# Performance work log

Measured on AMD Instinct MI355X. Metric: run time of the kernel, lower is better.

## Reference

```python
import jax, jax.numpy as jnp
import numpy as np

NH = 32
LN_EPS = 1e-5

def _mlp2(x, w1, b1, w2, b2):
    # Linear -> ReLU -> Linear (torch convention: y = x @ W^T + b)
    return jnp.maximum(x @ w1.T + b1, 0.0) @ w2.T + b2

def _layernorm(x, g, b):
    m = x.mean(-1, keepdims=True)
    v = jnp.mean((x - m) ** 2, axis=-1, keepdims=True)
    return (x - m) / jnp.sqrt(v + LN_EPS) * g + b

def _pos_enc(pos):
    # P[..., 2i] = sin(pos/(i+1)*pi), P[..., 2i+1] = cos(pos/(i+1)*pi)
    i = jnp.arange(NH // 2, dtype=pos.dtype)
    ang = pos[..., None] * (jnp.pi / (i + 1.0))  # [B, L, NH/2]
    return jnp.stack([jnp.sin(ang), jnp.cos(ang)], axis=-1).reshape(pos.shape[0], pos.shape[1], NH)

def _forward(x0, x1, pos0, pos1, xcT,
             e0w1, e0b1, e0w2, e0b2,
             e1w1, e1b1, e1w2, e1b2,
             ecw1, ecb1, ecw2, ecb2,
             wq, wk, wv, wo,
             ln1g, ln1b, ln2g, ln2b,
             f1w1, f1b1, f1w2, f1b2,
             f2w1, f2b1, f2w2, f2b2,
             l0, l1):
    # InputFeature
    e0 = _mlp2(x0, e0w1, e0b1, e0w2, e0b2) + _pos_enc(pos0)      # [B, l0, 32]
    e1 = _mlp2(x1, e1w1, e1b1, e1w2, e1b2) + _pos_enc(pos1)      # [B, l1, 32]
    ec = _mlp2(xcT, ecw1, ecb1, ecw2, ecb2)                      # [B, 32]
    xIn = jnp.concatenate([e0, e1, ec[:, None, :]], axis=1)      # [B, L, 32], L = l0+l1+1
    # AttentionLayer: attention over the feature axis (faithful to bmm(q^T, k))
    q = xIn @ wq.T; k = xIn @ wk.T; v = xIn @ wv.T               # [B, L, 32]
    L = xIn.shape[1]
    score = jnp.einsum('blh,blg->bhg', q, k) / jnp.sqrt(jnp.asarray(L, xIn.dtype))  # [B, 32, 32]
    att = jax.nn.softmax(score, axis=-1)
    a = jnp.einsum('bhg,blg->blh', att, v) @ wo.T                # [B, L, 32]
    # addnorm1 (dropout in eval = identity) + ffn1 + addnorm2 + ffn2
    h1 = _layernorm(a + xIn, ln1g, ln1b)
    h2 = _mlp2(h1, f1w1, f1b1, f1w2, f1b2)
    h3 = _layernorm(h2 + xIn, ln2g, ln2b)
    y = _mlp2(h3, f2w1, f2b1, f2w2, f2b2)[..., 0]                # [B, L]
    # segment-mean pooling: sum of per-segment means (last segment = xc token)
    return y[:, :l0].mean(-1) + y[:, l0:l0 + l1].mean(-1) + y[:, l0 + l1:].mean(-1)

def setup_inputs() -> dict:
    key = jax.random.key(0)
    ks = iter(jax.random.split(key, 48))
    B, L0, L1, N0, N1, NXC = 2048, 365, 366, 8, 16, 32
    lin = lambda o, i: jax.random.normal(next(ks), (o, i), jnp.float32) * np.float32(1.0 / np.sqrt(i))
    d = {}
    d['x0'] = jax.random.normal(next(ks), (B, L0, N0), jnp.float32)
    d['x1'] = jax.random.normal(next(ks), (B, L1, N1), jnp.float32)
    d['pos0'] = jax.random.uniform(next(ks), (B, L0), jnp.float32) * 365.0
    d['pos1'] = jax.random.uniform(next(ks), (B, L1), jnp.float32) * 365.0
    d['xcT'] = jax.random.normal(next(ks), (B, NXC), jnp.float32)
    d['e0w1'] = lin(NH, N0); d['e0b1'] = jnp.zeros((NH,), jnp.float32)
    d['e0w2'] = lin(NH, NH); d['e0b2'] = jnp.zeros((NH,), jnp.float32)
    d['e1w1'] = lin(NH, N1); d['e1b1'] = jnp.zeros((NH,), jnp.float32)
    d['e1w2'] = lin(NH, NH); d['e1b2'] = jnp.zeros((NH,), jnp.float32)
    d['ecw1'] = lin(NH, NXC); d['ecb1'] = jnp.zeros((NH,), jnp.float32)
    d['ecw2'] = lin(NH, NH); d['ecb2'] = jnp.zeros((NH,), jnp.float32)
    d['wq'] = lin(NH, NH); d['wk'] = lin(NH, NH); d['wv'] = lin(NH, NH); d['wo'] = lin(NH, NH)
    d['ln1g'] = jnp.ones((NH,), jnp.float32); d['ln1b'] = jnp.zeros((NH,), jnp.float32)
    d['ln2g'] = jnp.ones((NH,), jnp.float32); d['ln2b'] = jnp.zeros((NH,), jnp.float32)
    d['f1w1'] = lin(NH, NH); d['f1b1'] = jnp.zeros((NH,), jnp.float32)
    d['f1w2'] = lin(NH, NH); d['f1b2'] = jnp.zeros((NH,), jnp.float32)
    d['f2w1'] = lin(NH, NH); d['f2b1'] = jnp.zeros((NH,), jnp.float32)
    d['f2w2'] = lin(1, NH); d['f2b2'] = jnp.zeros((1,), jnp.float32)
    d['l0'] = L0; d['l1'] = L1
    return d

def reference(x0, x1, pos0, pos1, xcT,
              e0w1, e0b1, e0w2, e0b2, e1w1, e1b1, e1w2, e1b2,
              ecw1, ecb1, ecw2, ecb2, wq, wk, wv, wo,
              ln1g, ln1b, ln2g, ln2b,
              f1w1, f1b1, f1w2, f1b2, f2w1, f2b1, f2w2, f2b2,
              l0, l1):
    return _forward(x0, x1, pos0, pos1, xcT,
                    e0w1, e0b1, e0w2, e0b2, e1w1, e1b1, e1w2, e1b2,
                    ecw1, ecb1, ecw2, ecb2, wq, wk, wv, wo,
                    ln1g, ln1b, ln2g, ln2b,
                    f1w1, f1b1, f1w2, f1b2, f2w1, f2b1, f2w2, f2b2,
                    l0, l1)
```

## Files before the change

kernel.cpp:

```cpp
#include <hip/hip_runtime.h>
#include <math.h>

#define L0T 365
#define L1T 366
#define LT  732
#define NTILE 46
#define NW   4
#define NTHR 256
#define PI_F 3.14159265358979323846f

typedef short svec8 __attribute__((ext_vector_type(8)));
typedef float fvec4 __attribute__((ext_vector_type(4)));
typedef float fvec16 __attribute__((ext_vector_type(16)));
typedef unsigned uvec4 __attribute__((ext_vector_type(4)));

__device__ __forceinline__ unsigned short f2bf(float f) {
    unsigned u = __float_as_uint(f);
    u = (u + 0x7fffu + ((u >> 16) & 1u)) >> 16;
    return (unsigned short)u;
}
__device__ __forceinline__ float bf2f(unsigned short s) {
    return __uint_as_float(((unsigned)s) << 16);
}
__device__ __forceinline__ unsigned pk2(float a, float b) {
    return (unsigned)f2bf(a) | ((unsigned)f2bf(b) << 16);
}
__device__ __forceinline__ unsigned cvtpk(float a, float b) {
    unsigned r;
    asm("v_cvt_pk_bf16_f32 %0, %1, %2" : "=v"(r) : "v"(a), "v"(b));
    return r;
}
__device__ __forceinline__ float pgetv(uvec4 p, int j) {
    unsigned u = p[j >> 1];
    return bf2f((unsigned short)((j & 1) ? (u >> 16) : (u & 0xffffu)));
}
__device__ __forceinline__ svec8 pack8(float4 a, float4 c) {
    uvec4 u;
    u[0] = cvtpk(a.x, a.y); u[1] = cvtpk(a.z, a.w);
    u[2] = cvtpk(c.x, c.y); u[3] = cvtpk(c.z, c.w);
    return __builtin_bit_cast(svec8, u);
}

__device__ __forceinline__ void embed_pass(
    const unsigned short* __restrict__ T1,
    const unsigned short* __restrict__ T2,
    const float* __restrict__ Bh, const float* __restrict__ Bx,
    svec8 bx, int ln, int Q, float* __restrict__ out)
{
    svec8 w1f0 = *(const svec8*)&T1[ln * 8];
    svec8 w1f1 = *(const svec8*)&T1[512 + ln * 8];
    const fvec4* bh = (const fvec4*)&Bh[Q * 8];
    fvec4 d0 = __builtin_amdgcn_mfma_f32_16x16x32_bf16(w1f0, bx, bh[0], 0, 0, 0);
    fvec4 d1 = __builtin_amdgcn_mfma_f32_16x16x32_bf16(w1f1, bx, bh[1], 0, 0, 0);
    uvec4 hu;
    hu[0] = cvtpk(fmaxf(d0[0], 0.f), fmaxf(d0[1], 0.f));
    hu[1] = cvtpk(fmaxf(d0[2], 0.f), fmaxf(d0[3], 0.f));
    hu[2] = cvtpk(fmaxf(d1[0], 0.f), fmaxf(d1[1], 0.f));
    hu[3] = cvtpk(fmaxf(d1[2], 0.f), fmaxf(d1[3], 0.f));
    svec8 hf = __builtin_bit_cast(svec8, hu);
    svec8 w2f0 = *(const svec8*)&T2[ln * 8];
    svec8 w2f1 = *(const svec8*)&T2[512 + ln * 8];
    const fvec4* bb = (const fvec4*)&Bx[Q * 8];
    fvec4 g0 = __builtin_amdgcn_mfma_f32_16x16x32_bf16(w2f0, hf, bb[0], 0, 0, 0);
    fvec4 g1 = __builtin_amdgcn_mfma_f32_16x16x32_bf16(w2f1, hf, bb[1], 0, 0, 0);
    out[0] = g0[0]; out[1] = g0[1]; out[2] = g0[2]; out[3] = g0[3];
    out[4] = g1[0]; out[5] = g1[1]; out[6] = g1[2]; out[7] = g1[3];
}

__device__ __forceinline__ void embed_tile(
    int t, int b, int tk, int Q, int ln,
    const float* __restrict__ x0, const float* __restrict__ x1,
    const float* __restrict__ pos0, const float* __restrict__ pos1,
    const unsigned short* __restrict__ TBL,
    const float* __restrict__ BIA,
    float4 pwr,
    const float* __restrict__ ECV,
    float* __restrict__ xv)
{
    const float pwa[4] = {pwr.x, pwr.y, pwr.z, pwr.w};
    const int tok = t * 16 + tk;
    if (t < 22) {
        svec8 bx;
        #pragma unroll
        for (int j = 0; j < 8; j++) bx[j] = 0;
        if (Q == 0) {
            const float4* px = (const float4*)(x0 + ((size_t)b * L0T + tok) * 8);
            bx = pack8(px[0], px[1]);
        }
        embed_pass(TBL, TBL + 1024, BIA, BIA + 32, bx, ln, Q, xv);
        float pv = pos0[(size_t)b * L0T + tok];
        #pragma unroll
        for (int j = 0; j < 8; j += 2) {
            float s, c; __sincosf(pv * pwa[j >> 1], &s, &c);
            xv[j] += s; xv[j + 1] += c;
        }
    } else if (t == 22) {
        float ea[8], eb[8];
        svec8 bx0, bx1;
        #pragma unroll
        for (int j = 0; j < 8; j++) { bx0[j] = 0; bx1[j] = 0; }
        if (Q == 0 && tok < L0T) {
            const float4* px = (const float4*)(x0 + ((size_t)b * L0T + tok) * 8);
            bx0 = pack8(px[0], px[1]);
        }
        if (Q < 2 && tok >= L0T) {
            const float4* px = (const float4*)(x1 + ((size_t)b * L1T + (tok - L0T)) * 16 + Q * 8);
            bx1 = pack8(px[0], px[1]);
        }
        embed_pass(TBL,        TBL + 1024, BIA,      BIA + 32, bx0, ln, Q, ea);
        embed_pass(TBL + 2048, TBL + 3072, BIA + 64, BIA + 96, bx1, ln, Q, eb);
        float pv = (tok < L0T) ? pos0[(size_t)b * L0T + tok]
                               : pos1[(size_t)b * L1T + (tok - L0T)];
        #pragma unroll
        for (int j = 0; j < 8; j += 2) {
            float s, c; __sincosf(pv * pwa[j >> 1], &s, &c);
            xv[j]     = ((tok < L0T) ? ea[j]     : eb[j])     + s;
            xv[j + 1] = ((tok < L0T) ? ea[j + 1] : eb[j + 1]) + c;
        }
    } else if (t < 45) {
        svec8 bx;
        #pragma unroll
        for (int j = 0; j < 8; j++) bx[j] = 0;
        if (Q < 2) {
            const float4* px = (const float4*)(x1 + ((size_t)b * L1T + (tok - L0T)) * 16 + Q * 8);
            bx = pack8(px[0], px[1]);
        }
        embed_pass(TBL + 2048, TBL + 3072, BIA + 64, BIA + 96, bx, ln, Q, xv);
        float pv = pos1[(size_t)b * L1T + (tok - L0T)];
        #pragma unroll
        for (int j = 0; j < 8; j += 2) {
            float s, c; __sincosf(pv * pwa[j >> 1], &s, &c);
            xv[j] += s; xv[j + 1] += c;
        }
    } else {
        float ea[8];
        svec8 bx1;
        #pragma unroll
        for (int j = 0; j < 8; j++) bx1[j] = 0;
        if (Q < 2 && tok <= LT - 2) {
            const float4* px = (const float4*)(x1 + ((size_t)b * L1T + (tok - L0T)) * 16 + Q * 8);
            bx1 = pack8(px[0], px[1]);
        }
        embed_pass(TBL + 2048, TBL + 3072, BIA + 64, BIA + 96, bx1, ln, Q, ea);
        float pv = (tok <= LT - 2) ? pos1[(size_t)b * L1T + (tok - L0T)] : 0.f;
        #pragma unroll
        for (int j = 0; j < 8; j += 2) {
            float s, c; __sincosf(pv * pwa[j >> 1], &s, &c);
            xv[j]     = (tok <= LT - 2) ? ea[j] + s
                        : ((tok == LT - 1) ? ECV[Q * 8 + j] : 0.f);
            xv[j + 1] = (tok <= LT - 2) ? ea[j + 1] + c
                        : ((tok == LT - 1) ? ECV[Q * 8 + j + 1] : 0.f);
        }
    }
}

__global__ __launch_bounds__(NTHR, 6) void fused_kernel(
    const float* __restrict__ x0,  const float* __restrict__ x1,
    const float* __restrict__ pos0,const float* __restrict__ pos1,
    const float* __restrict__ xcT,
    const float* __restrict__ e0w1,const float* __restrict__ e0b1,
    const float* __restrict__ e0w2,const float* __restrict__ e0b2,
    const float* __restrict__ e1w1,const float* __restrict__ e1b1,
    const float* __restrict__ e1w2,const float* __restrict__ e1b2,
    const float* __restrict__ ecw1,const float* __restrict__ ecb1,
    const float* __restrict__ ecw2,const float* __restrict__ ecb2,
    const float* __restrict__ wq,  const float* __restrict__ wk,
    const float* __restrict__ wv,  const float* __restrict__ wo,
    const float* __restrict__ ln1g,const float* __restrict__ ln1b,
    const float* __restrict__ ln2g,const float* __restrict__ ln2b,
    const float* __restrict__ f1w1,const float* __restrict__ f1b1,
    const float* __restrict__ f1w2,const float* __restrict__ f1b2,
    const float* __restrict__ f2w1,const float* __restrict__ f2b1,
    const float* __restrict__ f2w2,const float* __restrict__ f2b2,
    float* __restrict__ out)
{
    const int b   = blockIdx.x;
    const int tid = threadIdx.x;
    const int w   = tid >> 6;
    const int ln  = tid & 63;
    const int tk  = ln & 15;
    const int Q   = ln >> 4;
    const int Lr0 = ((tk >> 2) * 8) + (tk & 3);
    const int Lr1 = Lr0 + 4;

    __shared__ unsigned short TBL[4 * 1024] __attribute__((aligned(16)));
    __shared__ float BIA[128] __attribute__((aligned(16)));
    __shared__ unsigned PCK[128] __attribute__((aligned(16)));
    __shared__ float T1f[1024] __attribute__((aligned(16)));
    __shared__ float CmT2[1024] __attribute__((aligned(16)));
    __shared__ unsigned short Wbb[1024] __attribute__((aligned(16)));
    __shared__ float ECV[32] __attribute__((aligned(16)));
    __shared__ float red[NW * 3];

    float4 pwr;
    pwr.x = PI_F / (float)(Q * 4 + 1);
    pwr.y = PI_F / (float)(Q * 4 + 2);
    pwr.z = PI_F / (float)(Q * 4 + 3);
    pwr.w = PI_F / (float)(Q * 4 + 4);

    for (int idx = tid; idx < 1024; idx += NTHR) {
        int f = idx >> 9, lane = (idx >> 3) & 63, j = idx & 7;
        int tkk = lane & 15, QQ = lane >> 4;
        int Lr = ((tkk >> 2) * 8) + (tkk & 3) + f * 4;
        int col = QQ * 8 + j;
        TBL[idx]        = (col < 8)  ? f2bf(e0w1[Lr * 8  + col]) : (unsigned short)0;
        TBL[1024 + idx] = f2bf(e0w2[Lr * 32 + col]);
        TBL[2048 + idx] = (col < 16) ? f2bf(e1w1[Lr * 16 + col]) : (unsigned short)0;
        TBL[3072 + idx] = f2bf(e1w2[Lr * 32 + col]);
        CmT2[idx] = 0.f;
    }
    if (tid < 128) {
        int s = tid >> 5, i = tid & 31;
        float bv;
        if      (s == 0) bv = e0b1[i];
        else if (s == 1) bv = e0b2[i];
        else if (s == 2) bv = e1b1[i];
        else             bv = e1b2[i];
        BIA[tid] = bv;
    }
    if (tid < 128) {
        int t8 = tid >> 4, q = (tid >> 2) & 3, i = tid & 3, f = q * 8 + 2 * i;
        const float* sp;
        if      (t8 == 0) sp = ln1g;
        else if (t8 == 1) sp = ln1b;
        else if (t8 == 2) sp = ln2g;
        else if (t8 == 3) sp = ln2b;
        else if (t8 == 4) sp = f1b1;
        else if (t8 == 5) sp = f1b2;
        else if (t8 == 6) sp = f2b1;
        else              sp = f2w2;
        PCK[tid] = pk2(sp[f], sp[f + 1]);
    }
    float* ECH = T1f;
    if (tid >= 224) {
        int i = tid - 224;
        const float4* xr = (const float4*)(xcT + (size_t)b * 32);
        const float4* wr = (const float4*)&ecw1[i * 32];
        float a = ecb1[i];
        #pragma unroll
        for (int j4 = 0; j4 < 8; j4++) {
            float4 ww = wr[j4], xx = xr[j4];
            a = fmaf(ww.x, xx.x, a); a = fmaf(ww.y, xx.y, a);
            a = fmaf(ww.z, xx.z, a); a = fmaf(ww.w, xx.w, a);
        }
        ECH[i] = fmaxf(a, 0.f);
    }
    __syncthreads();
    if (tid >= 224) {
        int i = tid - 224;
        const float4* wr = (const float4*)&ecw2[i * 32];
        float a = ecb2[i];
        #pragma unroll
        for (int j4 = 0; j4 < 8; j4++) {
            float4 ww = wr[j4];
            a = fmaf(ww.x, ECH[j4 * 4 + 0], a); a = fmaf(ww.y, ECH[j4 * 4 + 1], a);
            a = fmaf(ww.z, ECH[j4 * 4 + 2], a); a = fmaf(ww.w, ECH[j4 * 4 + 3], a);
        }
        ECV[i] = a;
    }
    __syncthreads();

    {
        unsigned short* ST = (unsigned short*)T1f;
        const int feat = ln & 31, half = ln >> 5;
        fvec16 dG;
        #pragma unroll
        for (int i = 0; i < 16; i++) dG[i] = 0.f;
        for (int t = w; t < NTILE; t += NW) {
            float xv[8];
            embed_tile(t, b, tk, Q, ln, x0, x1, pos0, pos1, TBL, BIA, pwr, ECV, xv);
            uvec4 pk;
            pk[0] = cvtpk(xv[0], xv[1]); pk[1] = cvtpk(xv[2], xv[3]);
            pk[2] = cvtpk(xv[4], xv[5]); pk[3] = cvtpk(xv[6], xv[7]);
            *(uvec4*)&ST[(w * 16 + tk) * 32 + Q * 8] = pk;
            svec8 af;
            #pragma unroll
            for (int j = 0; j < 8; j++)
                af[j] = (short)ST[w * 512 + (half * 8 + j) * 32 + feat];
            dG = __builtin_amdgcn_mfma_f32_32x32x16_bf16(af, af, dG, 0, 0, 0);
        }
        #pragma unroll
        for (int rg = 0; rg < 16; rg++) {
            int row = (rg & 3) + 8 * (rg >> 2) + 4 * half;
            atomicAdd(&CmT2[row * 32 + feat], dG[rg]);
        }
    }
    __syncthreads();

    for (int idx = tid; idx < 1024; idx += NTHR) {
        int i = idx >> 5, g = idx & 31;
        const float4* cr = (const float4*)&CmT2[i * 32];
        const float4* wr = (const float4*)&wk[g * 32];
        float a = 0.f;
        #pragma unroll
        for (int j4 = 0; j4 < 8; j4++) {
            float4 cc = cr[j4], ww = wr[j4];
            a = fmaf(cc.x, ww.x, a); a = fmaf(cc.y, ww.y, a);
            a = fmaf(cc.z, ww.z, a); a = fmaf(cc.w, ww.w, a);
        }
        T1f[idx] = a;
    }
    __syncthreads();
    const float rsL = rsqrtf((float)LT);
    for (int idx = tid; idx < 1024; idx += NTHR) {
        int h = idx >> 5, g = idx & 31;
        const float4* qr = (const float4*)&wq[h * 32];
        float a = 0.f;
        #pragma unroll
        for (int i4 = 0; i4 < 8; i4++) {
            float4 qq = qr[i4];
            a = fmaf(qq.x, T1f[(i4 * 4 + 0) * 32 + g], a);
            a = fmaf(qq.y, T1f[(i4 * 4 + 1) * 32 + g], a);
            a = fmaf(qq.z, T1f[(i4 * 4 + 2) * 32 + g], a);
            a = fmaf(qq.w, T1f[(i4 * 4 + 3) * 32 + g], a);
        }
        CmT2[idx] = a * rsL;
    }
    __syncthreads();
    {
        int r = tid >> 3, c0 = (tid & 7) * 4;
        float4 vv = *(const float4*)&CmT2[r * 32 + c0];
        float m = fmaxf(fmaxf(vv.x, vv.y), fmaxf(vv.z, vv.w));
        m = fmaxf(m, __shfl_xor(m, 1));
        m = fmaxf(m, __shfl_xor(m, 2));
        m = fmaxf(m, __shfl_xor(m, 4));
        float ex = __expf(vv.x - m), ey = __expf(vv.y - m);
        float ez = __expf(vv.z - m), ew = __expf(vv.w - m);
        float s = ex + ey + ez + ew;
        s += __shfl_xor(s, 1); s += __shfl_xor(s, 2); s += __shfl_xor(s, 4);
        float inv = 1.f / s;
        float4 o; o.x = ex * inv; o.y = ey * inv; o.z = ez * inv; o.w = ew * inv;
        *(float4*)&CmT2[r * 32 + c0] = o;
    }
    __syncthreads();
    for (int idx = tid; idx < 1024; idx += NTHR) {
        int h = idx >> 5, j = idx & 31;
        const float4* pr = (const float4*)&CmT2[h * 32];
        float a = 0.f;
        #pragma unroll
        for (int g4 = 0; g4 < 8; g4++) {
            float4 pp = pr[g4];
            a = fmaf(pp.x, wv[(g4 * 4 + 0) * 32 + j], a);
            a = fmaf(pp.y, wv[(g4 * 4 + 1) * 32 + j], a);
            a = fmaf(pp.z, wv[(g4 * 4 + 2) * 32 + j], a);
            a = fmaf(pp.w, wv[(g4 * 4 + 3) * 32 + j], a);
        }
        T1f[idx] = a;
    }
    __syncthreads();
    for (int idx = tid; idx < 1024; idx += NTHR) {
        int o = idx >> 5, j = idx & 31;
        const float4* orow = (const float4*)&wo[o * 32];
        float a = 0.f;
        #pragma unroll
        for (int h4 = 0; h4 < 8; h4++) {
            float4 oo = orow[h4];
            a = fmaf(oo.x, T1f[(h4 * 4 + 0) * 32 + j], a);
            a = fmaf(oo.y, T1f[(h4 * 4 + 1) * 32 + j], a);
            a = fmaf(oo.z, T1f[(h4 * 4 + 2) * 32 + j], a);
            a = fmaf(oo.w, T1f[(h4 * 4 + 3) * 32 + j], a);
        }
        Wbb[idx] = f2bf(a + (o == j ? 1.f : 0.f));
    }
    __syncthreads();

    svec8 wbf0 = *(const svec8*)&Wbb[Lr0 * 32 + Q * 8];
    svec8 wbf1 = *(const svec8*)&Wbb[Lr1 * 32 + Q * 8];
    svec8 a1f0, a1f1, a2f0, a2f1, a3f0, a3f1;
    #pragma unroll
    for (int j = 0; j < 8; j++) {
        a1f0[j] = (short)f2bf(f1w1[Lr0 * 32 + Q * 8 + j]);
        a1f1[j] = (short)f2bf(f1w1[Lr1 * 32 + Q * 8 + j]);
        a2f0[j] = (short)f2bf(f1w2[Lr0 * 32 + Q * 8 + j]);
        a2f1[j] = (short)f2bf(f1w2[Lr1 * 32 + Q * 8 + j]);
        a3f0[j] = (short)f2bf(f2w1[Lr0 * 32 + Q * 8 + j]);
        a3f1[j] = (short)f2bf(f2w1[Lr1 * 32 + Q * 8 + j]);
    }
    const float ybias = f2b2[0];
    const fvec4 zc = {0.f, 0.f, 0.f, 0.f};

    float s0 = 0.f, s1 = 0.f, s2 = 0.f;
    for (int t = w; t < NTILE; t += NW) {
        float xv[8];
        embed_tile(t, b, tk, Q, ln, x0, x1, pos0, pos1, TBL, BIA, pwr, ECV, xv);
        uvec4 pkx;
        pkx[0] = cvtpk(xv[0], xv[1]); pkx[1] = cvtpk(xv[2], xv[3]);
        pkx[2] = cvtpk(xv[4], xv[5]); pkx[3] = cvtpk(xv[6], xv[7]);
        svec8 bx = __builtin_bit_cast(svec8, pkx);

        const uvec4* P4 = (const uvec4*)PCK;
        uvec4 pg1 = P4[Q],      pb1 = P4[4 + Q];
        uvec4 pg2 = P4[8 + Q],  pb2 = P4[12 + Q];
        uvec4 pc1 = P4[16 + Q], pc2 = P4[20 + Q];
        uvec4 pc3 = P4[24 + Q], pw2 = P4[28 + Q];

        fvec4 d0 = __builtin_amdgcn_mfma_f32_16x16x32_bf16(wbf0, bx, zc, 0, 0, 0);
        fvec4 d1 = __builtin_amdgcn_mfma_f32_16x16x32_bf16(wbf1, bx, zc, 0, 0, 0);
        float v[8];
        #pragma unroll
        for (int j = 0; j < 4; j++) { v[j] = d0[j]; v[4 + j] = d1[j]; }
        float S = 0.f, Sq = 0.f;
        #pragma unroll
        for (int j = 0; j < 8; j++) { S += v[j]; Sq = fmaf(v[j], v[j], Sq); }
        S  += __shfl_xor(S, 16);  Sq += __shfl_xor(Sq, 16);
        S  += __shfl_xor(S, 32);  Sq += __shfl_xor(Sq, 32);
        float mean = S * (1.f / 32.f);
        float var = fmaxf(Sq * (1.f / 32.f) - mean * mean, 0.f);
        float rs = rsqrtf(var + 1e-5f);
        float n[8];
        #pragma unroll
        for (int j = 0; j < 8; j++)
            n[j] = (v[j] - mean) * rs * pgetv(pg1, j) + pgetv(pb1, j);
        uvec4 tu;
        tu[0] = cvtpk(n[0], n[1]); tu[1] = cvtpk(n[2], n[3]);
        tu[2] = cvtpk(n[4], n[5]); tu[3] = cvtpk(n[6], n[7]);
        svec8 tf = __builtin_bit_cast(svec8, tu);
        fvec4 u0 = __builtin_amdgcn_mfma_f32_16x16x32_bf16(a1f0, tf, zc, 0, 0, 0);
        fvec4 u1 = __builtin_amdgcn_mfma_f32_16x16x32_bf16(a1f1, tf, zc, 0, 0, 0);
        uvec4 uu;
        uu[0] = cvtpk(fmaxf(u0[0] + pgetv(pc1, 0), 0.f), fmaxf(u0[1] + pgetv(pc1, 1), 0.f));
        uu[1] = cvtpk(fmaxf(u0[2] + pgetv(pc1, 2), 0.f), fmaxf(u0[3] + pgetv(pc1, 3), 0.f));
        uu[2] = cvtpk(fmaxf(u1[0] + pgetv(pc1, 4), 0.f), fmaxf(u1[1] + pgetv(pc1, 5), 0.f));
        uu[3] = cvtpk(fmaxf(u1[2] + pgetv(pc1, 6), 0.f), fmaxf(u1[3] + pgetv(pc1, 7), 0.f));
        svec8 uf = __builtin_bit_cast(svec8, uu);
        fvec4 g0 = __builtin_amdgcn_mfma_f32_16x16x32_bf16(a2f0, uf, zc, 0, 0, 0);
        fvec4 g1 = __builtin_amdgcn_mfma_f32_16x16x32_bf16(a2f1, uf, zc, 0, 0, 0);
        #pragma unroll
        for (int j = 0; j < 8; j++)
            v[j] = (j < 4 ? g0[j] : g1[j - 4]) + pgetv(pc2, j) + xv[j];
        float S2 = 0.f, Sq2 = 0.f;
        #pragma unroll
        for (int j = 0; j < 8; j++) { S2 += v[j]; Sq2 = fmaf(v[j], v[j], Sq2); }
        S2  += __shfl_xor(S2, 16);  Sq2 += __shfl_xor(Sq2, 16);
        S2  += __shfl_xor(S2, 32);  Sq2 += __shfl_xor(Sq2, 32);
        float mean2 = S2 * (1.f / 32.f);
        float var2 = fmaxf(Sq2 * (1.f / 32.f) - mean2 * mean2, 0.f);
        float rs2 = rsqrtf(var2 + 1e-5f);
        float n2[8];
        #pragma unroll
        for (int j = 0; j < 8; j++)
            n2[j] = (v[j] - mean2) * rs2 * pgetv(pg2, j) + pgetv(pb2, j);
        uvec4 t2u;
        t2u[0] = cvtpk(n2[0], n2[1]); t2u[1] = cvtpk(n2[2], n2[3]);
        t2u[2] = cvtpk(n2[4], n2[5]); t2u[3] = cvtpk(n2[6], n2[7]);
        svec8 t2 = __builtin_bit_cast(svec8, t2u);
        fvec4 q0 = __builtin_amdgcn_mfma_f32_16x16x32_bf16(a3f0, t2, zc, 0, 0, 0);
        fvec4 q1 = __builtin_amdgcn_mfma_f32_16x16x32_bf16(a3f1, t2, zc, 0, 0, 0);
        float yp = 0.f;
        #pragma unroll
        for (int j = 0; j < 8; j++) {
            float e = (j < 4 ? q0[j] : q1[j - 4]) + pgetv(pc3, j);
            yp = fmaf(pgetv(pw2, j), fmaxf(e, 0.f), yp);
        }
        yp += __shfl_xor(yp, 16); yp += __shfl_xor(yp, 32);
        if (Q == 0) {
            int tok = t * 16 + tk;
            float yv = yp + ybias;
            if (tok < L0T)            s0 += yv;
            else if (tok < LT - 1)    s1 += yv;
            else if (tok == LT - 1)   s2 += yv;
        }
    }

    s0 += __shfl_xor(s0, 1); s0 += __shfl_xor(s0, 2);
    s0 += __shfl_xor(s0, 4); s0 += __shfl_xor(s0, 8);
    s1 += __shfl_xor(s1, 1); s1 += __shfl_xor(s1, 2);
    s1 += __shfl_xor(s1, 4); s1 += __shfl_xor(s1, 8);
    s2 += __shfl_xor(s2, 1); s2 += __shfl_xor(s2, 2);
    s2 += __shfl_xor(s2, 4); s2 += __shfl_xor(s2, 8);
    if (ln == 0) { red[w * 3] = s0; red[w * 3 + 1] = s1; red[w * 3 + 2] = s2; }
    __syncthreads();
    if (tid == 0) {
        float a0 = 0.f, a1 = 0.f, a2 = 0.f;
        #pragma unroll
        for (int k = 0; k < NW; k++) {
            a0 += red[k * 3]; a1 += red[k * 3 + 1]; a2 += red[k * 3 + 2];
        }
        out[b] = a0 / (float)L0T + a1 / (float)L1T + a2;
    }
}

extern "C" void kernel_launch(void* const* d_in, const int* in_sizes, int n_in,
                              void* d_out, int out_size, void* d_ws, size_t ws_size,
                              hipStream_t stream)
{
    const float* x0   = (const float*)d_in[0];
    const float* x1   = (const float*)d_in[1];
    const float* pos0 = (const float*)d_in[2];
    const float* pos1 = (const float*)d_in[3];
    const float* xcT  = (const float*)d_in[4];
    const float* e0w1 = (const float*)d_in[5];
    const float* e0b1 = (const float*)d_in[6];
    const float* e0w2 = (const float*)d_in[7];
    const float* e0b2 = (const float*)d_in[8];
    const float* e1w1 = (const float*)d_in[9];
    const float* e1b1 = (const float*)d_in[10];
    const float* e1w2 = (const float*)d_in[11];
    const float* e1b2 = (const float*)d_in[12];
    const float* ecw1 = (const float*)d_in[13];
    const float* ecb1 = (const float*)d_in[14];
    const float* ecw2 = (const float*)d_in[15];
    const float* ecb2 = (const float*)d_in[16];
    const float* wq   = (const float*)d_in[17];
    const float* wk   = (const float*)d_in[18];
    const float* wv   = (const float*)d_in[19];
    const float* wo   = (const float*)d_in[20];
    const float* ln1g = (const float*)d_in[21];
    const float* ln1b = (const float*)d_in[22];
    const float* ln2g = (const float*)d_in[23];
    const float* ln2b = (const float*)d_in[24];
    const float* f1w1 = (const float*)d_in[25];
    const float* f1b1 = (const float*)d_in[26];
    const float* f1w2 = (const float*)d_in[27];
    const float* f1b2 = (const float*)d_in[28];
    const float* f2w1 = (const float*)d_in[29];
    const float* f2b1 = (const float*)d_in[30];
    const float* f2w2 = (const float*)d_in[31];
    const float* f2b2 = (const float*)d_in[32];
    float* out = (float*)d_out;

    const int B = in_sizes[0] / (L0T * 8);

    hipLaunchKernelGGL(fused_kernel, dim3(B), dim3(NTHR), 0, stream,
                       x0, x1, pos0, pos1, xcT,
                       e0w1, e0b1, e0w2, e0b2, e1w1, e1b1, e1w2, e1b2,
                       ecw1, ecb1, ecw2, ecb2, wq, wk, wv, wo,
                       ln1g, ln1b, ln2g, ln2b,
                       f1w1, f1b1, f1w2, f1b2, f2w1, f2b1, f2w2, f2b2,
                       out);
}
```

Baseline: 325.2 us.

## Split token tiles per segment and process two tiles per iteration for ILP

Re-tiles the token axis so each 16-token tile belongs to one segment (x0 or x1, with the xc token placed at the end of segment 1). This removes the mixed boundary tile that ran both embedding MLPs. Both the Gram pass and the main per-token pipeline now handle two tiles per loop iteration, issuing loads and MFMA chains side by side so their latencies can overlap; the Gram pass uses two accumulators. Occupancy in launch bounds drops from 6 to 4 to make room for the extra registers, which may reduce latency hiding across waves.

```diff
diff --git a/kernel.cpp b/kernel.cpp
--- a/kernel.cpp
+++ b/kernel.cpp
@@ -5,6 +5,7 @@
 #define L1T 366
 #define LT  732
 #define NTILE 46
+#define NSEG 23
 #define NW   4
 #define NTHR 256
 #define PI_F 3.14159265358979323846f
@@ -67,94 +68,47 @@
     out[4] = g1[0]; out[5] = g1[1]; out[6] = g1[2]; out[7] = g1[3];
 }
 
-__device__ __forceinline__ void embed_tile(
-    int t, int b, int tk, int Q, int ln,
+__device__ __forceinline__ void load_tile(
+    int t, int b, int tk, int Q,
     const float* __restrict__ x0, const float* __restrict__ x1,
     const float* __restrict__ pos0, const float* __restrict__ pos1,
-    const unsigned short* __restrict__ TBL,
-    const float* __restrict__ BIA,
-    float4 pwr,
-    const float* __restrict__ ECV,
-    float* __restrict__ xv)
+    svec8& bx, float& pv, int& seg, int& tl)
 {
+    seg = (t >= NSEG) ? 1 : 0;
+    tl  = (seg ? (t - NSEG) : t) * 16 + tk;
+    const int lim = seg ? L1T : L0T;
+    const bool tvalid = tl < lim;
+    #pragma unroll
+    for (int j = 0; j < 8; j++) bx[j] = 0;
+    const bool ld = tvalid && (seg ? (Q < 2) : (Q == 0));
+    if (ld) {
+        const float4* px = seg
+            ? (const float4*)(x1 + ((size_t)b * L1T + tl) * 16 + Q * 8)
+            : (const float4*)(x0 + ((size_t)b * L0T + tl) * 8);
+        bx = pack8(px[0], px[1]);
+    }
+    pv = 0.f;
+    if (tvalid) pv = seg ? pos1[(size_t)b * L1T + tl] : pos0[(size_t)b * L0T + tl];
+}
+
+__device__ __forceinline__ void finish_xv(
+    int seg, int tl, int Q, const float* __restrict__ e, float pv, float4 pwr,
+    const float* __restrict__ ECV, float* __restrict__ xv)
+{
+    const int lim = seg ? L1T : L0T;
+    const bool tvalid = tl < lim;
+    const bool isxc = seg && (tl == L1T);
     const float pwa[4] = {pwr.x, pwr.y, pwr.z, pwr.w};
-    const int tok = t * 16 + tk;
-    if (t < 22) {
-        svec8 bx;
-        #pragma unroll
-        for (int j = 0; j < 8; j++) bx[j] = 0;
-        if (Q == 0) {
-            const float4* px = (const float4*)(x0 + ((size_t)b * L0T + tok) * 8);
-            bx = pack8(px[0], px[1]);
-        }
-        embed_pass(TBL, TBL + 1024, BIA, BIA + 32, bx, ln, Q, xv);
-        float pv = pos0[(size_t)b * L0T + tok];
-        #pragma unroll
-        for (int j = 0; j < 8; j += 2) {
-            float s, c; __sincosf(pv * pwa[j >> 1], &s, &c);
-            xv[j] += s; xv[j + 1] += c;
-        }
-    } else if (t == 22) {
-        float ea[8], eb[8];
-        svec8 bx0, bx1;
-        #pragma unroll
-        for (int j = 0; j < 8; j++) { bx0[j] = 0; bx1[j] = 0; }
-        if (Q == 0 && tok < L0T) {
-            const float4* px = (const float4*)(x0 + ((size_t)b * L0T + tok) * 8);
-            bx0 = pack8(px[0], px[1]);
-        }
-        if (Q < 2 && tok >= L0T) {
-            const float4* px = (const float4*)(x1 + ((size_t)b * L1T + (tok - L0T)) * 16 + Q * 8);
-            bx1 = pack8(px[0], px[1]);
-        }
-        embed_pass(TBL,        TBL + 1024, BIA,      BIA + 32, bx0, ln, Q, ea);
-        embed_pass(TBL + 2048, TBL + 3072, BIA + 64, BIA + 96, bx1, ln, Q, eb);
-        float pv = (tok < L0T) ? pos0[(size_t)b * L0T + tok]
-                               : pos1[(size_t)b * L1T + (tok - L0T)];
-        #pragma unroll
-        for (int j = 0; j < 8; j += 2) {
-            float s, c; __sincosf(pv * pwa[j >> 1], &s, &c);
-            xv[j]     = ((tok < L0T) ? ea[j]     : eb[j])     + s;
-            xv[j + 1] = ((tok < L0T) ? ea[j + 1] : eb[j + 1]) + c;
-        }
-    } else if (t < 45) {
-        svec8 bx;
-        #pragma unroll
-        for (int j = 0; j < 8; j++) bx[j] = 0;
-        if (Q < 2) {
-            const float4* px = (const float4*)(x1 + ((size_t)b * L1T + (tok - L0T)) * 16 + Q * 8);
-            bx = pack8(px[0], px[1]);
-        }
-        embed_pass(TBL + 2048, TBL + 3072, BIA + 64, BIA + 96, bx, ln, Q, xv);
-        float pv = pos1[(size_t)b * L1T + (tok - L0T)];
-        #pragma unroll
-        for (int j = 0; j < 8; j += 2) {
-            float s, c; __sincosf(pv * pwa[j >> 1], &s, &c);
-            xv[j] += s; xv[j + 1] += c;
-        }
-    } else {
-        float ea[8];
-        svec8 bx1;
-        #pragma unroll
-        for (int j = 0; j < 8; j++) bx1[j] = 0;
-        if (Q < 2 && tok <= LT - 2) {
-            const float4* px = (const float4*)(x1 + ((size_t)b * L1T + (tok - L0T)) * 16 + Q * 8);
-            bx1 = pack8(px[0], px[1]);
-        }
-        embed_pass(TBL + 2048, TBL + 3072, BIA + 64, BIA + 96, bx1, ln, Q, ea);
-        float pv = (tok <= LT - 2) ? pos1[(size_t)b * L1T + (tok - L0T)] : 0.f;
-        #pragma unroll
-        for (int j = 0; j < 8; j += 2) {
-            float s, c; __sincosf(pv * pwa[j >> 1], &s, &c);
-            xv[j]     = (tok <= LT - 2) ? ea[j] + s
-                        : ((tok == LT - 1) ? ECV[Q * 8 + j] : 0.f);
-            xv[j + 1] = (tok <= LT - 2) ? ea[j + 1] + c
-                        : ((tok == LT - 1) ? ECV[Q * 8 + j + 1] : 0.f);
-        }
-    }
-}
-
-__global__ __launch_bounds__(NTHR, 6) void fused_kernel(
+    #pragma unroll
+    for (int j = 0; j < 8; j += 2) {
+        float s, c; __sincosf(pv * pwa[j >> 1], &s, &c);
+        float a0 = e[j] + s, a1 = e[j + 1] + c;
+        xv[j]     = tvalid ? a0 : (isxc ? ECV[Q * 8 + j]     : 0.f);
+        xv[j + 1] = tvalid ? a1 : (isxc ? ECV[Q * 8 + j + 1] : 0.f);
+    }
+}
+
+__global__ __launch_bounds__(NTHR, 4) void fused_kernel(
     const float* __restrict__ x0,  const float* __restrict__ x1,
     const float* __restrict__ pos0,const float* __restrict__ pos1,
     const float* __restrict__ xcT,
@@ -186,11 +140,13 @@
     __shared__ unsigned short TBL[4 * 1024] __attribute__((aligned(16)));
     __shared__ float BIA[128] __attribute__((aligned(16)));
     __shared__ unsigned PCK[128] __attribute__((aligned(16)));
-    __shared__ float T1f[1024] __attribute__((aligned(16)));
-    __shared__ float CmT2[1024] __attribute__((aligned(16)));
+    __shared__ float SCR[2048] __attribute__((aligned(16)));
     __shared__ unsigned short Wbb[1024] __attribute__((aligned(16)));
     __shared__ float ECV[32] __attribute__((aligned(16)));
     __shared__ float red[NW * 3];
+
+    float* T1f  = SCR;
+    float* CmT2 = SCR + 1024;
 
     float4 pwr;
     pwr.x = PI_F / (float)(Q * 4 + 1);
@@ -260,15 +216,21 @@
     }
     __syncthreads();
 
+    const int cnt = (NTILE - 1 - w) / NW + 1;
+
     {
         unsigned short* ST = (unsigned short*)T1f;
         const int feat = ln & 31, half = ln >> 5;
-        fvec16 dG;
-        #pragma unroll
-        for (int i = 0; i < 16; i++) dG[i] = 0.f;
-        for (int t = w; t < NTILE; t += NW) {
-            float xv[8];
-            embed_tile(t, b, tk, Q, ln, x0, x1, pos0, pos1, TBL, BIA, pwr, ECV, xv);
+        fvec16 dGA, dGB;
+        #pragma unroll
+        for (int i = 0; i < 16; i++) { dGA[i] = 0.f; dGB[i] = 0.f; }
+
+        auto embed_core = [&](int seg, svec8 bx, float* e) {
+            const unsigned short* T = TBL + seg * 2048;
+            const float* Bb = BIA + seg * 64;
+            embed_pass(T, T + 1024, Bb, Bb + 32, bx, ln, Q, e);
+        };
+        auto gram_step = [&](const float* xv, fvec16& dG) {
             uvec4 pk;
             pk[0] = cvtpk(xv[0], xv[1]); pk[1] = cvtpk(xv[2], xv[3]);
             pk[2] = cvtpk(xv[4], xv[5]); pk[3] = cvtpk(xv[6], xv[7]);
@@ -278,11 +240,36 @@
             for (int j = 0; j < 8; j++)
                 af[j] = (short)ST[w * 512 + (half * 8 + j) * 32 + feat];
             dG = __builtin_amdgcn_mfma_f32_32x32x16_bf16(af, af, dG, 0, 0, 0);
-        }
+        };
+        auto g_one = [&](int t) {
+            svec8 bx; float pv; int seg, tl;
+            load_tile(t, b, tk, Q, x0, x1, pos0, pos1, bx, pv, seg, tl);
+            float e[8]; embed_core(seg, bx, e);
+            float xv[8]; finish_xv(seg, tl, Q, e, pv, pwr, ECV, xv);
+            gram_step(xv, dGA);
+        };
+        auto g_pair = [&](int tA, int tB) {
+            svec8 bxA, bxB; float pvA, pvB; int segA, tlA, segB, tlB;
+            load_tile(tA, b, tk, Q, x0, x1, pos0, pos1, bxA, pvA, segA, tlA);
+            load_tile(tB, b, tk, Q, x0, x1, pos0, pos1, bxB, pvB, segB, tlB);
+            float eA[8], eB[8];
+            embed_core(segA, bxA, eA);
+            embed_core(segB, bxB, eB);
+            float xvA[8], xvB[8];
+            finish_xv(segA, tlA, Q, eA, pvA, pwr, ECV, xvA);
+            finish_xv(segB, tlB, Q, eB, pvB, pwr, ECV, xvB);
+            gram_step(xvA, dGA);
+            gram_step(xvB, dGB);
+        };
+
+        int ts = w;
+        if (cnt & 1) { g_one(ts); ts += NW; }
+        for (int t = ts; t < NTILE; t += 2 * NW) g_pair(t, t + NW);
+
         #pragma unroll
         for (int rg = 0; rg < 16; rg++) {
             int row = (rg & 3) + 8 * (rg >> 2) + 4 * half;
-            atomicAdd(&CmT2[row * 32 + feat], dG[rg]);
+            atomicAdd(&CmT2[row * 32 + feat], dGA[rg] + dGB[rg]);
         }
     }
     __syncthreads();
@@ -378,88 +365,122 @@
     }
     const float ybias = f2b2[0];
     const fvec4 zc = {0.f, 0.f, 0.f, 0.f};
+    const uvec4* P4 = (const uvec4*)PCK;
 
     float s0 = 0.f, s1 = 0.f, s2 = 0.f;
-    for (int t = w; t < NTILE; t += NW) {
-        float xv[8];
-        embed_tile(t, b, tk, Q, ln, x0, x1, pos0, pos1, TBL, BIA, pwr, ECV, xv);
-        uvec4 pkx;
-        pkx[0] = cvtpk(xv[0], xv[1]); pkx[1] = cvtpk(xv[2], xv[3]);
-        pkx[2] = cvtpk(xv[4], xv[5]); pkx[3] = cvtpk(xv[6], xv[7]);
-        svec8 bx = __builtin_bit_cast(svec8, pkx);
-
-        const uvec4* P4 = (const uvec4*)PCK;
-        uvec4 pg1 = P4[Q],      pb1 = P4[4 + Q];
-        uvec4 pg2 = P4[8 + Q],  pb2 = P4[12 + Q];
-        uvec4 pc1 = P4[16 + Q], pc2 = P4[20 + Q];
-        uvec4 pc3 = P4[24 + Q], pw2 = P4[28 + Q];
-
-        fvec4 d0 = __builtin_amdgcn_mfma_f32_16x16x32_bf16(wbf0, bx, zc, 0, 0, 0);
-        fvec4 d1 = __builtin_amdgcn_mfma_f32_16x16x32_bf16(wbf1, bx, zc, 0, 0, 0);
-        float v[8];
-        #pragma unroll
-        for (int j = 0; j < 4; j++) { v[j] = d0[j]; v[4 + j] = d1[j]; }
-        float S = 0.f, Sq = 0.f;
-        #pragma unroll
-        for (int j = 0; j < 8; j++) { S += v[j]; Sq = fmaf(v[j], v[j], Sq); }
-        S  += __shfl_xor(S, 16);  Sq += __shfl_xor(Sq, 16);
-        S  += __shfl_xor(S, 32);  Sq += __shfl_xor(Sq, 32);
-        float mean = S * (1.f / 32.f);
-        float var = fmaxf(Sq * (1.f / 32.f) - mean * mean, 0.f);
-        float rs = rsqrtf(var + 1e-5f);
-        float n[8];
-        #pragma unroll
-        for (int j = 0; j < 8; j++)
-            n[j] = (v[j] - mean) * rs * pgetv(pg1, j) + pgetv(pb1, j);
-        uvec4 tu;
-        tu[0] = cvtpk(n[0], n[1]); tu[1] = cvtpk(n[2], n[3]);
-        tu[2] = cvtpk(n[4], n[5]); tu[3] = cvtpk(n[6], n[7]);
-        svec8 tf = __builtin_bit_cast(svec8, tu);
-        fvec4 u0 = __builtin_amdgcn_mfma_f32_16x16x32_bf16(a1f0, tf, zc, 0, 0, 0);
-        fvec4 u1 = __builtin_amdgcn_mfma_f32_16x16x32_bf16(a1f1, tf, zc, 0, 0, 0);
-        uvec4 uu;
-        uu[0] = cvtpk(fmaxf(u0[0] + pgetv(pc1, 0), 0.f), fmaxf(u0[1] + pgetv(pc1, 1), 0.f));
-        uu[1] = cvtpk(fmaxf(u0[2] + pgetv(pc1, 2), 0.f), fmaxf(u0[3] + pgetv(pc1, 3), 0.f));
-        uu[2] = cvtpk(fmaxf(u1[0] + pgetv(pc1, 4), 0.f), fmaxf(u1[1] + pgetv(pc1, 5), 0.f));
-        uu[3] = cvtpk(fmaxf(u1[2] + pgetv(pc1, 6), 0.f), fmaxf(u1[3] + pgetv(pc1, 7), 0.f));
-        svec8 uf = __builtin_bit_cast(svec8, uu);
-        fvec4 g0 = __builtin_amdgcn_mfma_f32_16x16x32_bf16(a2f0, uf, zc, 0, 0, 0);
-        fvec4 g1 = __builtin_amdgcn_mfma_f32_16x16x32_bf16(a2f1, uf, zc, 0, 0, 0);
-        #pragma unroll
-        for (int j = 0; j < 8; j++)
-            v[j] = (j < 4 ? g0[j] : g1[j - 4]) + pgetv(pc2, j) + xv[j];
-        float S2 = 0.f, Sq2 = 0.f;
-        #pragma unroll
-        for (int j = 0; j < 8; j++) { S2 += v[j]; Sq2 = fmaf(v[j], v[j], Sq2); }
-        S2  += __shfl_xor(S2, 16);  Sq2 += __shfl_xor(Sq2, 16);
-        S2  += __shfl_xor(S2, 32);  Sq2 += __shfl_xor(Sq2, 32);
-        float mean2 = S2 * (1.f / 32.f);
-        float var2 = fmaxf(Sq2 * (1.f / 32.f) - mean2 * mean2, 0.f);
-        float rs2 = rsqrtf(var2 + 1e-5f);
-        float n2[8];
-        #pragma unroll
-        for (int j = 0; j < 8; j++)
-            n2[j] = (v[j] - mean2) * rs2 * pgetv(pg2, j) + pgetv(pb2, j);
-        uvec4 t2u;
-        t2u[0] = cvtpk(n2[0], n2[1]); t2u[1] = cvtpk(n2[2], n2[3]);
-        t2u[2] = cvtpk(n2[4], n2[5]); t2u[3] = cvtpk(n2[6], n2[7]);
-        svec8 t2 = __builtin_bit_cast(svec8, t2u);
-        fvec4 q0 = __builtin_amdgcn_mfma_f32_16x16x32_bf16(a3f0, t2, zc, 0, 0, 0);
-        fvec4 q1 = __builtin_amdgcn_mfma_f32_16x16x32_bf16(a3f1, t2, zc, 0, 0, 0);
-        float yp = 0.f;
-        #pragma unroll
-        for (int j = 0; j < 8; j++) {
-            float e = (j < 4 ? q0[j] : q1[j - 4]) + pgetv(pc3, j);
-            yp = fmaf(pgetv(pw2, j), fmaxf(e, 0.f), yp);
-        }
-        yp += __shfl_xor(yp, 16); yp += __shfl_xor(yp, 32);
-        if (Q == 0) {
-            int tok = t * 16 + tk;
-            float yv = yp + ybias;
-            if (tok < L0T)            s0 += yv;
-            else if (tok < LT - 1)    s1 += yv;
-            else if (tok == LT - 1)   s2 += yv;
-        }
+    {
+        auto embed_core = [&](int seg, svec8 bx, float* e) {
+            const unsigned short* T = TBL + seg * 2048;
+            const float* Bb = BIA + seg * 64;
+            embed_pass(T, T + 1024, Bb, Bb + 32, bx, ln, Q, e);
+        };
+        auto pipe_rest = [&](const float* xv) -> float {
+            uvec4 pkx;
+            pkx[0] = cvtpk(xv[0], xv[1]); pkx[1] = cvtpk(xv[2], xv[3]);
+            pkx[2] = cvtpk(xv[4], xv[5]); pkx[3] = cvtpk(xv[6], xv[7]);
+            svec8 bx = __builtin_bit_cast(svec8, pkx);
+            fvec4 d0 = __builtin_amdgcn_mfma_f32_16x16x32_bf16(wbf0, bx, zc, 0, 0, 0);
+            fvec4 d1 = __builtin_amdgcn_mfma_f32_16x16x32_bf16(wbf1, bx, zc, 0, 0, 0);
+            float v[8];
+            #pragma unroll
+            for (int j = 0; j < 4; j++) { v[j] = d0[j]; v[4 + j] = d1[j]; }
+            float S = 0.f, Sq = 0.f;
+            #pragma unroll
+            for (int j = 0; j < 8; j++) { S += v[j]; Sq = fmaf(v[j], v[j], Sq); }
+            S  += __shfl_xor(S, 16);  Sq += __shfl_xor(Sq, 16);
+            S  += __shfl_xor(S, 32);  Sq += __shfl_xor(Sq, 32);
+            float mean = S * (1.f / 32.f);
+            float var = fmaxf(Sq * (1.f / 32.f) - mean * mean, 0.f);
+            float rs = rsqrtf(var + 1e-5f);
+            uvec4 pg1 = P4[Q], pb1 = P4[4 + Q];
+            float n[8];
+            #pragma unroll
+            for (int j = 0; j < 8; j++)
+                n[j] = (v[j] - mean) * rs * pgetv(pg1, j) + pgetv(pb1, j);
+            uvec4 tu;
+            tu[0] = cvtpk(n[0], n[1]); tu[1] = cvtpk(n[2], n[3]);
+            tu[2] = cvtpk(n[4], n[5]); tu[3] = cvtpk(n[6], n[7]);
+            svec8 tf = __builtin_bit_cast(svec8, tu);
+            fvec4 u0 = __builtin_amdgcn_mfma_f32_16x16x32_bf16(a1f0, tf, zc, 0, 0, 0);
+            fvec4 u1 = __builtin_amdgcn_mfma_f32_16x16x32_bf16(a1f1, tf, zc, 0, 0, 0);
+            uvec4 pc1 = P4[16 + Q];
+            uvec4 uu;
+            uu[0] = cvtpk(fmaxf(u0[0] + pgetv(pc1, 0), 0.f), fmaxf(u0[1] + pgetv(pc1, 1), 0.f));
+            uu[1] = cvtpk(fmaxf(u0[2] + pgetv(pc1, 2), 0.f), fmaxf(u0[3] + pgetv(pc1, 3), 0.f));
+            uu[2] = cvtpk(fmaxf(u1[0] + pgetv(pc1, 4), 0.f), fmaxf(u1[1] + pgetv(pc1, 5), 0.f));
+            uu[3] = cvtpk(fmaxf(u1[2] + pgetv(pc1, 6), 0.f), fmaxf(u1[3] + pgetv(pc1, 7), 0.f));
+            svec8 uf = __builtin_bit_cast(svec8, uu);
+            fvec4 g0 = __builtin_amdgcn_mfma_f32_16x16x32_bf16(a2f0, uf, zc, 0, 0, 0);
+            fvec4 g1 = __builtin_amdgcn_mfma_f32_16x16x32_bf16(a2f1, uf, zc, 0, 0, 0);
+            uvec4 pc2 = P4[20 + Q];
+            #pragma unroll
+            for (int j = 0; j < 8; j++)
+                v[j] = (j < 4 ? g0[j] : g1[j - 4]) + pgetv(pc2, j) + xv[j];
+            float S2 = 0.f, Sq2 = 0.f;
+            #pragma unroll
+            for (int j = 0; j < 8; j++) { S2 += v[j]; Sq2 = fmaf(v[j], v[j], Sq2); }
+            S2  += __shfl_xor(S2, 16);  Sq2 += __shfl_xor(Sq2, 16);
+            S2  += __shfl_xor(S2, 32);  Sq2 += __shfl_xor(Sq2, 32);
+            float mean2 = S2 * (1.f / 32.f);
+            float var2 = fmaxf(Sq2 * (1.f / 32.f) - mean2 * mean2, 0.f);
+            float rs2 = rsqrtf(var2 + 1e-5f);
+            uvec4 pg2 = P4[8 + Q], pb2 = P4[12 + Q];
+            float n2[8];
+            #pragma unroll
+            for (int j = 0; j < 8; j++)
+                n2[j] = (v[j] - mean2) * rs2 * pgetv(pg2, j) + pgetv(pb2, j);
+            uvec4 t2u;
+            t2u[0] = cvtpk(n2[0], n2[1]); t2u[1] = cvtpk(n2[2], n2[3]);
+            t2u[2] = cvtpk(n2[4], n2[5]); t2u[3] = cvtpk(n2[6], n2[7]);
+            svec8 t2 = __builtin_bit_cast(svec8, t2u);
+            fvec4 q0 = __builtin_amdgcn_mfma_f32_16x16x32_bf16(a3f0, t2, zc, 0, 0, 0);
+            fvec4 q1 = __builtin_amdgcn_mfma_f32_16x16x32_bf16(a3f1, t2, zc, 0, 0, 0);
+            uvec4 pc3 = P4[24 + Q], pw2 = P4[28 + Q];
+            float yp = 0.f;
+            #pragma unroll
+            for (int j = 0; j < 8; j++) {
+                float e = (j < 4 ? q0[j] : q1[j - 4]) + pgetv(pc3, j);
+                yp = fmaf(pgetv(pw2, j), fmaxf(e, 0.f), yp);
+            }
+            yp += __shfl_xor(yp, 16); yp += __shfl_xor(yp, 32);
+            return yp;
+        };
+        auto accum_y = [&](int seg, int tl, float yp) {
+            if (Q == 0) {
+                float yv = yp + ybias;
+                if (seg == 0) { if (tl < L0T) s0 += yv; }
+                else {
+                    if (tl < L1T)       s1 += yv;
+                    else if (tl == L1T) s2 += yv;
+                }
+            }
+        };
+        auto p_one = [&](int t) {
+            svec8 bx; float pv; int seg, tl;
+            load_tile(t, b, tk, Q, x0, x1, pos0, pos1, bx, pv, seg, tl);
+            float e[8]; embed_core(seg, bx, e);
+            float xv[8]; finish_xv(seg, tl, Q, e, pv, pwr, ECV, xv);
+            accum_y(seg, tl, pipe_rest(xv));
+        };
+        auto p_pair = [&](int tA, int tB) {
+            svec8 bxA, bxB; float pvA, pvB; int segA, tlA, segB, tlB;
+            load_tile(tA, b, tk, Q, x0, x1, pos0, pos1, bxA, pvA, segA, tlA);
+            load_tile(tB, b, tk, Q, x0, x1, pos0, pos1, bxB, pvB, segB, tlB);
+            float eA[8], eB[8];
+            embed_core(segA, bxA, eA);
+            embed_core(segB, bxB, eB);
+            float xvA[8], xvB[8];
+            finish_xv(segA, tlA, Q, eA, pvA, pwr, ECV, xvA);
+            finish_xv(segB, tlB, Q, eB, pvB, pwr, ECV, xvB);
+            float ypA = pipe_rest(xvA);
+            float ypB = pipe_rest(xvB);
+            accum_y(segA, tlA, ypA);
+            accum_y(segB, tlB, ypB);
+        };
+
+        int ts = w;
+        if (cnt & 1) { p_one(ts); ts += NW; }
+        for (int t = ts; t < NTILE; t += 2 * NW) p_pair(t, t + NW);
     }
 
     s0 += __shfl_xor(s0, 1); s0 += __shfl_xor(s0, 2);
```

Result: slower. 425.5 us (+30.8%).
